# Performance work log

Hardware: AMD Instinct MI355X
Metric: run time of the kernel (lower is better)

The kernel has to match this reference:

```python
import jax, jax.numpy as jnp
import numpy as np

NUM_HEADS = 16
D_MODEL = 1024
HEAD_DIM = D_MODEL // NUM_HEADS  # 64
BATCH = 2
SEQ = 2048
ROPE_THETA = 10000.0


def apply_rope(x, positions):
    # x: (B, S, H, hd), positions: (B, S) int
    hd = x.shape[-1]
    half = hd // 2
    inv_freq = 1.0 / (ROPE_THETA ** (jnp.arange(half, dtype=jnp.float32) / half))  # (half,)
    angles = positions[..., None].astype(jnp.float32) * inv_freq                   # (B, S, half)
    cos = jnp.cos(angles)[..., None, :]  # (B, S, 1, half) broadcast over heads
    sin = jnp.sin(angles)[..., None, :]
    x1, x2 = x[..., :half], x[..., half:]
    return jnp.concatenate([x1 * cos - x2 * sin, x1 * sin + x2 * cos], axis=-1).astype(x.dtype)


def setup_inputs() -> dict:
    key = jax.random.key(0)
    k1, k2, k3 = jax.random.split(key, 3)
    inputs = jax.random.normal(k1, (BATCH, SEQ, D_MODEL), dtype=jnp.float32)
    # Linear weights stored as (in, out); pytorch y = x @ W.T, equivalent math.
    w_in = jax.random.normal(k2, (D_MODEL, 3 * D_MODEL), dtype=jnp.float32) * (D_MODEL ** -0.5)
    w_out = jax.random.normal(k3, (D_MODEL, D_MODEL), dtype=jnp.float32) * (D_MODEL ** -0.5)
    positions = jnp.tile(jnp.arange(SEQ, dtype=jnp.int64)[None, :], (BATCH, 1))
    return {"inputs": inputs, "positions": positions, "w_in": w_in, "w_out": w_out}


def reference(inputs, positions, w_in, w_out):
    B, S, _ = inputs.shape
    # fused QKV projection; per-head layout is (heads, 3*head_dim) -> chunk into q,k,v
    proj = inputs @ w_in                                   # (B, S, 3*D)
    proj = proj.reshape(B, S, NUM_HEADS, 3 * HEAD_DIM)     # (B, S, H, 3*hd)
    q, k, v = jnp.split(proj, 3, axis=-1)                  # each (B, S, H, hd)
    q = apply_rope(q, positions)
    k = apply_rope(k, positions)
    # flex_attention with block_mask=None: full softmax attention, scale 1/sqrt(hd)
    scale = 1.0 / np.sqrt(HEAD_DIM)
    scores = jnp.einsum('bqhd,bkhd->bhqk', q, k) * scale   # (B, H, S, S)
    attn = jax.nn.softmax(scores, axis=-1)
    out = jnp.einsum('bhqk,bkhd->bqhd', attn, v)           # (B, S, H, hd)
    out = out.reshape(B, S, NUM_HEADS * HEAD_DIM)
    return out @ w_out                                     # (B, S, D)
```

## Files before the change

### kernel.cpp

```cpp
#include <hip/hip_runtime.h>

typedef float f32x4 __attribute__((ext_vector_type(4)));
typedef short s16x8 __attribute__((ext_vector_type(8)));
typedef unsigned short u16;

#define SQ 2048
#define DM 1024
#define NH 16
#define HD 64


__device__ __forceinline__ u16 f2bf(float f) {
    union { float f; unsigned u; } v; v.f = f;
    unsigned u = v.u + 0x7FFFu + ((v.u >> 16) & 1u);
    return (u16)(u >> 16);
}

__device__ __forceinline__ f32x4 mfma_bf16(s16x8 a, s16x8 b, f32x4 c) {
    asm("v_mfma_f32_16x16x32_bf16 %0, %1, %2, %0" : "+v"(c) : "v"(a), "v"(b));
    return c;
}

__device__ __forceinline__ void gload16(const void* g, const void* lds_base) {
    __builtin_amdgcn_global_load_lds(
        (const __attribute__((address_space(1))) unsigned int*)g,
        (__attribute__((address_space(3))) unsigned int*)lds_base,
        16, 0, 0);
}

__global__ void k_convert(const float* __restrict__ in, u16* __restrict__ out, int n4) {
    int i = blockIdx.x * blockDim.x + threadIdx.x;
    int stride = gridDim.x * blockDim.x;
    for (; i < n4; i += stride) {
        float4 f = ((const float4*)in)[i];
        ushort4 o;
        o.x = f2bf(f.x); o.y = f2bf(f.y); o.z = f2bf(f.z); o.w = f2bf(f.w);
        ((ushort4*)out)[i] = o;
    }
}

__global__ void k_transpose_bf16(const float* __restrict__ in, u16* __restrict__ out, int R, int C) {
    __shared__ float tile[32][33];
    int c0 = blockIdx.x * 32, r0 = blockIdx.y * 32;
    int tx = threadIdx.x, ty = threadIdx.y;
#pragma unroll
    for (int i = 0; i < 32; i += 8)
        tile[ty + i][tx] = in[(size_t)(r0 + ty + i) * C + c0 + tx];
    __syncthreads();
#pragma unroll
    for (int i = 0; i < 32; i += 8)
        out[(size_t)(c0 + ty + i) * R + r0 + tx] = f2bf(tile[tx][ty + i]);
}

__global__ void k_transpose_v(const u16* __restrict__ in, u16* __restrict__ out) {
    __shared__ u16 tile[32][33];
    int bh = blockIdx.z;
    int c0 = blockIdx.x * 32;
    int r0 = blockIdx.y * 32;
    const u16* src = in + (size_t)bh * SQ * HD;
    u16* dst = out + (size_t)bh * HD * SQ;
    int tx = threadIdx.x, ty = threadIdx.y;
#pragma unroll
    for (int i = 0; i < 32; i += 8)
        tile[ty + i][tx] = src[(size_t)(r0 + ty + i) * HD + c0 + tx];
    __syncthreads();
#pragma unroll
    for (int i = 0; i < 32; i += 8)
        dst[(size_t)(c0 + ty + i) * SQ + r0 + tx] = tile[tx][ty + i];
}

__global__ __launch_bounds__(256) void k_gemm_bt(
    const u16* __restrict__ A, const u16* __restrict__ Bt, float* __restrict__ C,
    int M, int N, int K)
{
    __shared__ u16 As[128 * 64];
    __shared__ u16 Bs[128 * 64];
    const int tid = threadIdx.x;
    const int lane = tid & 63;
    const int wave = tid >> 6;
    const int wr = wave >> 1, wc = wave & 1;
    const int m0 = blockIdx.y * 128, n0 = blockIdx.x * 128;
    const int l16 = lane & 15, g4 = lane >> 4;

    const int srow = lane >> 3;
    const int scol = (lane & 7) ^ srow;

    f32x4 acc[4][4] = {};

    for (int k0 = 0; k0 < K; k0 += 64) {
        __syncthreads();
#pragma unroll
        for (int j = 0; j < 4; ++j) {
            int rt = (wave * 4 + j) * 8 + srow;
            gload16(&A[(size_t)(m0 + rt) * K + k0 + scol * 8], &As[(wave * 4 + j) * 512]);
            gload16(&Bt[(size_t)(n0 + rt) * K + k0 + scol * 8], &Bs[(wave * 4 + j) * 512]);
        }
        __syncthreads();
#pragma unroll
        for (int kc = 0; kc < 2; ++kc) {
            s16x8 af[4], bfr[4];
#pragma unroll
            for (int i = 0; i < 4; ++i) {
                int ra = wr * 64 + i * 16 + l16;
                int offa = (kc * 64 + g4 * 16) ^ ((ra & 7) << 4);
                af[i] = *(const s16x8*)((const char*)As + ra * 128 + offa);
                int rb = wc * 64 + i * 16 + l16;
                int offb = (kc * 64 + g4 * 16) ^ ((rb & 7) << 4);
                bfr[i] = *(const s16x8*)((const char*)Bs + rb * 128 + offb);
            }
#pragma unroll
            for (int mi = 0; mi < 4; ++mi)
#pragma unroll
                for (int ni = 0; ni < 4; ++ni)
                    acc[mi][ni] = mfma_bf16(af[mi], bfr[ni], acc[mi][ni]);
        }
    }
    asm volatile("s_nop 7\ns_nop 7");
#pragma unroll
    for (int mi = 0; mi < 4; ++mi)
#pragma unroll
        for (int ni = 0; ni < 4; ++ni)
#pragma unroll
            for (int r = 0; r < 4; ++r) {
                int row = m0 + wr * 64 + mi * 16 + g4 * 4 + r;
                int col = n0 + wc * 64 + ni * 16 + l16;
                C[(size_t)row * N + col] = acc[mi][ni][r];
            }
}

__global__ __launch_bounds__(256) void k_gemm1_rope(
    const u16* __restrict__ A, const u16* __restrict__ Bt,
    const int* __restrict__ positions,
    u16* __restrict__ Qb, u16* __restrict__ Kb, u16* __restrict__ Vb)
{
    const int M = 4096, N = 3072, K = 1024;
    __shared__ u16 As[128 * 64];
    __shared__ u16 Bs[128 * 64];
    const int tid = threadIdx.x;
    const int lane = tid & 63;
    const int wave = tid >> 6;
    const int wr = wave >> 1, wc = wave & 1;
    const int m0 = blockIdx.y * 128, n0 = blockIdx.x * 128;
    const int l16 = lane & 15, g4 = lane >> 4;

    const int srow = lane >> 3;
    const int scol = (lane & 7) ^ srow;

    f32x4 acc[4][4] = {};

    for (int k0 = 0; k0 < K; k0 += 64) {
        __syncthreads();
#pragma unroll
        for (int j = 0; j < 4; ++j) {
            int rt = (wave * 4 + j) * 8 + srow;
            gload16(&A[(size_t)(m0 + rt) * K + k0 + scol * 8], &As[(wave * 4 + j) * 512]);
            gload16(&Bt[(size_t)(n0 + rt) * K + k0 + scol * 8], &Bs[(wave * 4 + j) * 512]);
        }
        __syncthreads();
#pragma unroll
        for (int kc = 0; kc < 2; ++kc) {
            s16x8 af[4], bfr[4];
#pragma unroll
            for (int i = 0; i < 4; ++i) {
                int ra = wr * 64 + i * 16 + l16;
                int offa = (kc * 64 + g4 * 16) ^ ((ra & 7) << 4);
                af[i] = *(const s16x8*)((const char*)As + ra * 128 + offa);
                int rb = wc * 64 + i * 16 + l16;
                int offb = (kc * 64 + g4 * 16) ^ ((rb & 7) << 4);
                bfr[i] = *(const s16x8*)((const char*)Bs + rb * 128 + offb);
            }
#pragma unroll
            for (int mi = 0; mi < 4; ++mi)
#pragma unroll
                for (int ni = 0; ni < 4; ++ni)
                    acc[mi][ni] = mfma_bf16(af[mi], bfr[ni], acc[mi][ni]);
        }
    }
    asm volatile("s_nop 7\ns_nop 7");

#pragma unroll
    for (int mi = 0; mi < 4; ++mi)
#pragma unroll
        for (int r = 0; r < 4; ++r) {
            int row = m0 + wr * 64 + mi * 16 + g4 * 4 + r;
            int pos = positions[row];
            int b = row >> 11, s = row & (SQ - 1);
            float fpos = (float)pos;
#pragma unroll
            for (int ni = 0; ni < 4; ++ni) {
                float v = acc[mi][ni][r];
                int col = n0 + wc * 64 + ni * 16 + l16;
                int h = col / 192;
                int c = col - h * 192;
                int kind = c >> 6;
                int cc = c & 63;
                size_t o = (((size_t)(b * NH + h) * SQ + s)) * HD + cc;
                if (kind == 2) {
                    Vb[o] = f2bf(v);
                } else {
                    float partner = acc[mi][ni ^ 2][r];
                    int j = cc & 31;
                    int hi = cc >> 5;
                    float inv = __expf(-(float)j * (9.210340371976184f / 32.0f));
                    float sn, cs;
                    __sincosf(fpos * inv, &sn, &cs);
                    float x1 = hi ? partner : v;
                    float x2 = hi ? v : partner;
                    float outv = hi ? (x1 * sn + x2 * cs) : (x1 * cs - x2 * sn);
                    if (kind == 0) outv *= 0.125f;
                    (kind == 0 ? Qb : Kb)[o] = f2bf(outv);
                }
            }
        }
}

__global__ __launch_bounds__(256) void k_attn(
    const u16* __restrict__ Q, const u16* __restrict__ Kg, const u16* __restrict__ Vt,
    u16* __restrict__ O)
{
    __shared__ alignas(16) u16 Ks[64 * 64];
    __shared__ alignas(16) u16 Vs[64 * 64];
    __shared__ alignas(16) u16 Ps[4 * 16 * 72];
    const int tid = threadIdx.x, lane = tid & 63, wave = tid >> 6;
    const int bid = blockIdx.x;
    const int vb = (bid & 7) * 128 + (bid >> 3);
    const int bh = vb >> 5;
    const int q0 = (vb & 31) * 64;
    const int l16 = lane & 15, g4 = lane >> 4;
    const size_t base  = (size_t)bh * SQ * HD;
    const size_t vbase = (size_t)bh * HD * SQ;

    s16x8 qf[2];
    {
        const u16* qrow = Q + base + (size_t)(q0 + wave * 16 + l16) * HD + g4 * 8;
        qf[0] = *(const s16x8*)(qrow);
        qf[1] = *(const s16x8*)(qrow + 32);
    }
    f32x4 oacc[4] = {};
    f32x4 lsum = {0.f, 0.f, 0.f, 0.f};

    u16* Pw = Ps + wave * 16 * 72;
    const int r8 = lane >> 3, c8 = lane & 7;
    const int sw = c8 ^ r8;

    for (int t = 0; t < SQ / 64; ++t) {
        const int kk0 = t * 64;
        __syncthreads();
#pragma unroll
        for (int j = 0; j < 2; ++j) {
            int row = wave * 16 + j * 8 + r8;
            gload16(&Kg[base + (size_t)(kk0 + row) * HD + sw * 8],
                    &Ks[(wave * 16 + j * 8) * 64]);
            gload16(&Vt[vbase + (size_t)row * SQ + kk0 + sw * 8],
                    &Vs[(wave * 16 + j * 8) * 64]);
        }
        __syncthreads();

        f32x4 sacc[4] = {};
        __builtin_amdgcn_s_setprio(1);
#pragma unroll
        for (int kc = 0; kc < 2; ++kc)
#pragma unroll
            for (int ni = 0; ni < 4; ++ni) {
                int row = ni * 16 + l16;
                const char* p = (const char*)Ks + row * 128 +
                                ((kc * 64 + g4 * 16) ^ ((l16 & 7) << 4));
                sacc[ni] = mfma_bf16(qf[kc], *(const s16x8*)p, sacc[ni]);
            }
        __builtin_amdgcn_s_setprio(0);
        asm volatile("s_nop 7\ns_nop 7");

#pragma unroll
        for (int ni = 0; ni < 4; ++ni)
#pragma unroll
            for (int r = 0; r < 4; ++r) {
                float pv = __expf(sacc[ni][r]);
                lsum[r] += pv;
                Pw[(g4 * 4 + r) * 72 + ni * 16 + l16] = f2bf(pv);
            }

        __builtin_amdgcn_s_setprio(1);
#pragma unroll
        for (int kc = 0; kc < 2; ++kc) {
            s16x8 af = *(const s16x8*)(&Pw[l16 * 72 + kc * 32 + g4 * 8]);
#pragma unroll
            for (int di = 0; di < 4; ++di) {
                int row = di * 16 + l16;
                const char* p = (const char*)Vs + row * 128 +
                                ((kc * 64 + g4 * 16) ^ ((l16 & 7) << 4));
                oacc[di] = mfma_bf16(af, *(const s16x8*)p, oacc[di]);
            }
        }
        __builtin_amdgcn_s_setprio(0);
    }
    asm volatile("s_nop 7\ns_nop 7");

#pragma unroll
    for (int off = 1; off < 16; off <<= 1)
#pragma unroll
        for (int r = 0; r < 4; ++r) lsum[r] += __shfl_xor(lsum[r], off, 16);

    const int b = bh >> 4, h = bh & (NH - 1);
#pragma unroll
    for (int r = 0; r < 4; ++r) {
        float inv = 1.0f / lsum[r];
#pragma unroll
        for (int di = 0; di < 4; ++di) {
            int qrow = q0 + wave * 16 + g4 * 4 + r;
            O[((size_t)(b * SQ + qrow)) * DM + h * HD + di * 16 + l16] =
                f2bf(oacc[di][r] * inv);
        }
    }
}

extern "C" void kernel_launch(void* const* d_in, const int* in_sizes, int n_in,
                              void* d_out, int out_size, void* d_ws, size_t ws_size,
                              hipStream_t stream)
{
    const float* inputs    = (const float*)d_in[0];
    const int*   positions = (const int*)d_in[1];
    const float* w_in      = (const float*)d_in[2];
    const float* w_out     = (const float*)d_in[3];
    float* out = (float*)d_out;

    char* w = (char*)d_ws;
    u16* Vtb     = (u16*)(w);
    u16* inb     = (u16*)(w + 50331648);
    u16* winT    = (u16*)(w + 58720256);
    u16* woutT   = (u16*)(w + 65011712);
    u16* Qb      = (u16*)(w + 67108864);
    u16* Kb      = (u16*)(w + 75497472);
    u16* Vb      = (u16*)(w + 83886080);
    u16* attnb   = (u16*)(w + 92274688);

    k_convert<<<2048, 256, 0, stream>>>(inputs, inb, (4096 * 1024) / 4);
    k_transpose_bf16<<<dim3(96, 32), dim3(32, 8), 0, stream>>>(w_in, winT, 1024, 3072);
    k_transpose_bf16<<<dim3(32, 32), dim3(32, 8), 0, stream>>>(w_out, woutT, 1024, 1024);
    k_gemm1_rope<<<dim3(24, 32), 256, 0, stream>>>(inb, winT, positions, Qb, Kb, Vb);
    k_transpose_v<<<dim3(2, 64, 32), dim3(32, 8), 0, stream>>>(Vb, Vtb);
    k_attn<<<1024, 256, 0, stream>>>(Qb, Kb, Vtb, attnb);
    k_gemm_bt<<<dim3(8, 32), 256, 0, stream>>>(attnb, woutT, out, 4096, 1024, 1024);
}
```

Baseline: 140.1 us.

## Split attention over two KV halves with a separate combine kernel

The attention kernel now splits each query tile's key/value range into two halves, doubling the grid to 2048 blocks. Each block writes unnormalized fp32 partial outputs and row sums to workspace. A new combine kernel adds the two partials, normalizes them and converts to bf16 for the output projection. The aim is more parallelism and shorter per-block loops, paid for by extra fp32 partial traffic through global memory and one more kernel launch.

```diff
diff --git a/kernel.cpp b/kernel.cpp
--- a/kernel.cpp
+++ b/kernel.cpp
@@ -216,16 +216,18 @@
 
 __global__ __launch_bounds__(256) void k_attn(
     const u16* __restrict__ Q, const u16* __restrict__ Kg, const u16* __restrict__ Vt,
-    u16* __restrict__ O)
+    float* __restrict__ P0, float* __restrict__ P1,
+    float* __restrict__ L0, float* __restrict__ L1)
 {
     __shared__ alignas(16) u16 Ks[64 * 64];
     __shared__ alignas(16) u16 Vs[64 * 64];
     __shared__ alignas(16) u16 Ps[4 * 16 * 72];
     const int tid = threadIdx.x, lane = tid & 63, wave = tid >> 6;
     const int bid = blockIdx.x;
-    const int vb = (bid & 7) * 128 + (bid >> 3);
-    const int bh = vb >> 5;
-    const int q0 = (vb & 31) * 64;
+    const int vb = (bid & 7) * 256 + (bid >> 3);
+    const int bh = vb >> 6;
+    const int q0 = ((vb >> 1) & 31) * 64;
+    const int kt = vb & 1;
     const int l16 = lane & 15, g4 = lane >> 4;
     const size_t base  = (size_t)bh * SQ * HD;
     const size_t vbase = (size_t)bh * HD * SQ;
@@ -243,8 +245,8 @@
     const int r8 = lane >> 3, c8 = lane & 7;
     const int sw = c8 ^ r8;
 
-    for (int t = 0; t < SQ / 64; ++t) {
-        const int kk0 = t * 64;
+    for (int tt = 0; tt < 16; ++tt) {
+        const int kk0 = (kt * 16 + tt) * 64;
         __syncthreads();
 #pragma unroll
         for (int j = 0; j < 2; ++j) {
@@ -300,16 +302,42 @@
 #pragma unroll
         for (int r = 0; r < 4; ++r) lsum[r] += __shfl_xor(lsum[r], off, 16);
 
+    float* Op = kt ? P1 : P0;
+    float* Lp = kt ? L1 : L0;
     const int b = bh >> 4, h = bh & (NH - 1);
 #pragma unroll
     for (int r = 0; r < 4; ++r) {
-        float inv = 1.0f / lsum[r];
-#pragma unroll
-        for (int di = 0; di < 4; ++di) {
-            int qrow = q0 + wave * 16 + g4 * 4 + r;
-            O[((size_t)(b * SQ + qrow)) * DM + h * HD + di * 16 + l16] =
-                f2bf(oacc[di][r] * inv);
-        }
+        int qrow = q0 + wave * 16 + g4 * 4 + r;
+        if (l16 == 0) Lp[(size_t)bh * SQ + qrow] = lsum[r];
+#pragma unroll
+        for (int di = 0; di < 4; ++di)
+            Op[((size_t)(b * SQ + qrow)) * DM + h * HD + di * 16 + l16] = oacc[di][r];
+    }
+}
+
+__global__ __launch_bounds__(512) void k_combine(
+    const float* __restrict__ P0, const float* __restrict__ P1,
+    const float* __restrict__ L0, const float* __restrict__ L1,
+    u16* __restrict__ outb)
+{
+    int i = blockIdx.x * blockDim.x + threadIdx.x;
+    int stride = gridDim.x * blockDim.x;
+    const int n4 = 4096 * 1024 / 4;
+    for (; i < n4; i += stride) {
+        int row = i >> 8;
+        int col = (i & 255) * 4;
+        int b = row >> 11, s = row & (SQ - 1);
+        int h = col >> 6;
+        size_t li = (size_t)(b * NH + h) * SQ + s;
+        float inv = 1.0f / (L0[li] + L1[li]);
+        float4 a = ((const float4*)P0)[i];
+        float4 c = ((const float4*)P1)[i];
+        ushort4 o;
+        o.x = f2bf((a.x + c.x) * inv);
+        o.y = f2bf((a.y + c.y) * inv);
+        o.z = f2bf((a.z + c.z) * inv);
+        o.w = f2bf((a.w + c.w) * inv);
+        ((ushort4*)outb)[i] = o;
     }
 }
 
@@ -325,6 +353,10 @@
 
     char* w = (char*)d_ws;
     u16* Vtb     = (u16*)(w);
+    float* P0    = (float*)(w + 8388608);
+    float* P1    = (float*)(w + 25165824);
+    float* L0    = (float*)(w + 41943040);
+    float* L1    = (float*)(w + 42205184);
     u16* inb     = (u16*)(w + 50331648);
     u16* winT    = (u16*)(w + 58720256);
     u16* woutT   = (u16*)(w + 65011712);
@@ -338,6 +370,7 @@
     k_transpose_bf16<<<dim3(32, 32), dim3(32, 8), 0, stream>>>(w_out, woutT, 1024, 1024);
     k_gemm1_rope<<<dim3(24, 32), 256, 0, stream>>>(inb, winT, positions, Qb, Kb, Vb);
     k_transpose_v<<<dim3(2, 64, 32), dim3(32, 8), 0, stream>>>(Vb, Vtb);
-    k_attn<<<1024, 256, 0, stream>>>(Qb, Kb, Vtb, attnb);
+    k_attn<<<2048, 256, 0, stream>>>(Qb, Kb, Vtb, P0, P1, L0, L1);
+    k_combine<<<2048, 512, 0, stream>>>(P0, P1, L0, L1, attnb);
     k_gemm_bt<<<dim3(8, 32), 256, 0, stream>>>(attnb, woutT, out, 4096, 1024, 1024);
 }
```

Result: slower. 149.7 us (+6.9%).
